# Kernel optimization log

Hardware: AMD Instinct MI355X
Metric: run time of the kernel (lower is better)

Reference implementation:

```python
import jax, jax.numpy as jnp
import numpy as np

K, N, M, D = 64, 8192, 8, 32  # locations, time steps, covariate features, memory depth


def setup_inputs() -> dict:
    key = jax.random.key(0)
    ks = jax.random.split(key, 6)
    obs = jax.random.uniform(ks[0], (K, N), dtype=jnp.float32)            # event counts [K, N]
    covs = jax.random.normal(ks[1], (K, N, M), dtype=jnp.float32)          # covariates  [K, N, M]
    hbeta = jnp.array([2.0], dtype=jnp.float32)                            # decay rate param (torch init: 2)
    halpha = jax.random.uniform(ks[2], (K, K), dtype=jnp.float32) * 0.01   # excitation matrix, U(0, 0.01)
    gamma = jax.random.uniform(ks[3], (K,), dtype=jnp.float32) * 0.01      # covariate gate, U(0, 0.01)
    W1 = jax.random.normal(ks[4], (20, 2 * D * M), dtype=jnp.float32) * 0.05
    b1 = jnp.zeros((20,), dtype=jnp.float32)
    W2 = jax.random.normal(ks[5], (1, 20), dtype=jnp.float32) * 0.05
    b2 = jnp.zeros((1,), dtype=jnp.float32)
    return dict(obs=obs, covs=covs, hbeta=hbeta, halpha=halpha, gamma=gamma,
                W1=W1, b1=b1, W2=W2, b2=b2)


def _forward(obs, covs, hbeta, halpha, gamma, W1, b1, W2, b2):
    k, n = obs.shape
    beta = hbeta[0]
    decay = jnp.exp(-beta)

    # Excitation: S[t] = sum_{tp < t} obs[:, tp] * beta * exp(-(t - tp) * beta)
    # exact O(N) linear recurrence instead of the original per-t O(t) resummation.
    def step(S, o):
        return decay * (S + beta * o), S
    _, S_all = jax.lax.scan(step, jnp.zeros((k,), obs.dtype), obs.T)  # [N, K]
    lam1 = jax.nn.softplus(jnp.einsum('kj,nj->kn', halpha, S_all))     # [K, N] (hmu = 0 in subclass)

    # Edge-padded covariate windows: window at t is padded[:, t : t + 2D, :]
    padded = jnp.concatenate([
        jnp.repeat(covs[:, :1, :], D, axis=1),   # left pad with first step
        covs,
        jnp.repeat(covs[:, -1:, :], D, axis=1),  # right pad with last step
    ], axis=1)                                   # [K, N + 2D, M]
    idx = jnp.arange(n)[:, None] + jnp.arange(2 * D)[None, :]  # [N, 2D]
    X = padded[:, idx, :].reshape(k, n, 2 * D * M)             # [K, N, 2DM], time-major then M (matches torch reshape)

    # Tiny 2-layer MLP with softplus activations, vectorized over (K, N)
    h = jax.nn.softplus(jnp.einsum('knf,hf->knh', X, W1) + b1)           # [K, N, 20]
    mu = jax.nn.softplus(jnp.einsum('knh,oh->kno', h, W2) + b2)[..., 0]  # [K, N]

    lams = lam1 + gamma[:, None] * mu                                    # [K, N]
    loglik = jnp.sum(obs * jnp.log(lams) - lams)
    return loglik, lams


def reference(obs, covs, hbeta, halpha, gamma, W1, b1, W2, b2):
    return _forward(obs, covs, hbeta, halpha, gamma, W1, b1, W2, b2)
```

## Files before the change

kernel.cpp:

```cpp
#include <hip/hip_runtime.h>
#include <hip/hip_bf16.h>
#include <math.h>

#define KL 64
#define NT 8192
#define MF 8
#define DD 32
#define WIN 64
#define HD 20
#define HP 32
#define KF 512
#define NB 256
#define NXB (NT / NB)
#define NBLK (NXB * KL)
#define GRPS (KF / 8)
#define GROW 24
#define W1SZ (GRPS * GROW * 8)

typedef __attribute__((ext_vector_type(8))) short bf16x8;
typedef __attribute__((ext_vector_type(4))) float f32x4;

__device__ __forceinline__ float softplus_f(float x) {
    float e = __expf(-fabsf(x));
    return fmaxf(x, 0.0f) + __logf(1.0f + e);
}
__device__ __forceinline__ short f2bf(float x) {
    __hip_bfloat16 h = __float2bfloat16(x);
    return *reinterpret_cast<short*>(&h);
}

__global__ __launch_bounds__(256)
void pack_kernel(const float* __restrict__ W1, const float* __restrict__ b1,
                 const float* __restrict__ W2, short* __restrict__ W1b,
                 float* __restrict__ b1p, float* __restrict__ W2p) {
    int t = blockIdx.x * 256 + threadIdx.x;
    #pragma unroll
    for (int i = 0; i < 3; ++i) {
        int p = t + i * 4096;
        int e = p & 7;
        int rg = p >> 3;
        int r = rg % GROW;
        int grp = rg / GROW;
        W1b[p] = (r < HD) ? f2bf(W1[r * KF + grp * 8 + e]) : (short)0;
    }
    if (blockIdx.x == 0 && threadIdx.x < HP) {
        b1p[threadIdx.x] = (threadIdx.x < HD) ? b1[threadIdx.x] : 0.0f;
        W2p[threadIdx.x] = (threadIdx.x < HD) ? W2[threadIdx.x] : 0.0f;
    }
}

__global__ __launch_bounds__(256)
void mlp_mfma_kernel(const float* __restrict__ covs, const float* __restrict__ obs,
                     const float* __restrict__ halpha, const float* __restrict__ hbeta,
                     const short* __restrict__ W1b, const float* __restrict__ b1p,
                     const float* __restrict__ W2p, const float* __restrict__ b2,
                     const float* __restrict__ gamma, float* __restrict__ lams,
                     float* __restrict__ partial) {
    __shared__ short cov_s[(NB + WIN) * MF];
    __shared__ float T_s[NB + WIN];
    __shared__ float hsum[NB];
    __shared__ float wred[4];

    int k    = blockIdx.y;
    int n0   = blockIdx.x * NB;
    int tid  = threadIdx.x;
    int lane = tid & 63;
    int wave = tid >> 6;

    int n = n0 + tid;
    size_t idx = (size_t)k * NT + n;
    float obs_n = obs[idx];
    float beta  = hbeta[0];
    float gam   = gamma[k];
    float b2v   = b2[0];

    const float* cbase = covs + (size_t)k * NT * MF;
    for (int row = tid; row < NB + WIN; row += 256) {
        int tt = n0 - DD + row;
        tt = tt < 0 ? 0 : (tt > NT - 1 ? NT - 1 : tt);
        const float4* cp = (const float4*)(cbase + (size_t)tt * MF);
        float4 c0 = cp[0], c1 = cp[1];
        bf16x8 v;
        v[0] = f2bf(c0.x); v[1] = f2bf(c0.y); v[2] = f2bf(c0.z); v[3] = f2bf(c0.w);
        v[4] = f2bf(c1.x); v[5] = f2bf(c1.y); v[6] = f2bf(c1.z); v[7] = f2bf(c1.w);
        *(bf16x8*)&cov_s[row * MF] = v;
    }
    __syncthreads();

    int c = lane & 15;
    int g = lane >> 4;
    int wrow = wave * 64;

    f32x4 acc[4][2];
    #pragma unroll
    for (int mt = 0; mt < 4; ++mt) {
        acc[mt][0] = (f32x4){0.f, 0.f, 0.f, 0.f};
        acc[mt][1] = (f32x4){0.f, 0.f, 0.f, 0.f};
    }

    int r1 = (c < 4) ? (16 + c) : HD;
    const short* pB0 = W1b + g * (GROW * 8) + c * 8;
    const short* pB1 = W1b + g * (GROW * 8) + r1 * 8;
    const short* pA  = &cov_s[(wrow + c + g) * MF];

    const float* arow = halpha + (size_t)k * KL;
    int tA = n0 - WIN + tid;
    tA = tA < 0 ? 0 : tA;
    int tB = n0 + (NB - WIN) + wave * 16 + (lane & 15);
    float aA = 0.0f, aB = 0.0f;

    #pragma unroll 2
    for (int kk = 0; kk < KF / 32; ++kk) {
        #pragma unroll
        for (int jj = 0; jj < 4; ++jj) {
            int j = kk * 4 + jj;
            float aj = arow[j];
            const float* orow = obs + (size_t)j * NT;
            aA = fmaf(aj, orow[tA], aA);
            aB = fmaf(aj, orow[tB], aB);
        }
        bf16x8 b0  = *(const bf16x8*)(pB0 + kk * (4 * GROW * 8));
        bf16x8 b1v = *(const bf16x8*)(pB1 + kk * (4 * GROW * 8));
        #pragma unroll
        for (int mt = 0; mt < 4; ++mt) {
            bf16x8 a = *(const bf16x8*)(pA + (mt * 16 + kk * 4) * MF);
            acc[mt][0] = __builtin_amdgcn_mfma_f32_16x16x32_bf16(a, b0,  acc[mt][0], 0, 0, 0);
            acc[mt][1] = __builtin_amdgcn_mfma_f32_16x16x32_bf16(a, b1v, acc[mt][1], 0, 0, 0);
        }
    }
    T_s[tid] = aA;
    if (lane < 16) T_s[NB + wave * 16 + lane] = aB;

    float w2a = W2p[c],      b1a = b1p[c];
    float w2b = W2p[16 + c], b1b = b1p[16 + c];
    #pragma unroll
    for (int mt = 0; mt < 4; ++mt) {
        float rs[4];
        #pragma unroll
        for (int j = 0; j < 4; ++j) {
            float v = w2a * softplus_f(acc[mt][0][j] + b1a)
                    + w2b * softplus_f(acc[mt][1][j] + b1b);
            v += __shfl_xor(v, 1, 64);
            v += __shfl_xor(v, 2, 64);
            v += __shfl_xor(v, 4, 64);
            v += __shfl_xor(v, 8, 64);
            rs[j] = v;
        }
        if (c == 0)
            *(float4*)&hsum[wrow + mt * 16 + g * 4] = (float4){rs[0], rs[1], rs[2], rs[3]};
    }
    __syncthreads();

    float decay = __expf(-beta);
    int Lmax = (int)(30.0f / beta) + 2;
    float la = 0.0f;
    if (n0 > 0) {
        if (Lmax > WIN) Lmax = WIN;
        int it4 = (Lmax + 3) >> 2;
        float d2 = decay * decay;
        float d4 = d2 * d2;
        float w1 = beta * decay, w2 = w1 * decay, w3 = w2 * decay, w4 = w3 * decay;
        float la0 = 0.f, la1 = 0.f, la2 = 0.f, la3 = 0.f;
        const float* Tp = &T_s[tid + WIN];
        for (int it = 0; it < it4; ++it) {
            int i = it * 4;
            la0 = fmaf(w1, Tp[-(i + 1)], la0); w1 *= d4;
            la1 = fmaf(w2, Tp[-(i + 2)], la1); w2 *= d4;
            la2 = fmaf(w3, Tp[-(i + 3)], la2); w3 *= d4;
            la3 = fmaf(w4, Tp[-(i + 4)], la3); w4 *= d4;
        }
        la = (la0 + la1) + (la2 + la3);
    } else {
        if (Lmax > NT) Lmax = NT;
        float w = beta * decay;
        for (int i = 1; i <= Lmax; ++i) {
            if (i <= n) la = fmaf(w, T_s[tid + WIN - i], la);
            w *= decay;
        }
    }
    float lam1 = softplus_f(la);
    float mu = softplus_f(hsum[tid] + b2v);
    float lam = lam1 + gam * mu;
    lams[idx] = lam;
    float term = fmaf(obs_n, __logf(lam), -lam);

    #pragma unroll
    for (int off = 32; off > 0; off >>= 1) term += __shfl_down(term, off, 64);
    if ((tid & 63) == 0) wred[tid >> 6] = term;
    __syncthreads();
    if (tid == 0)
        partial[blockIdx.y * gridDim.x + blockIdx.x] =
            (wred[0] + wred[1]) + (wred[2] + wred[3]);
}

__global__ __launch_bounds__(256)
void finalize_kernel(const float* __restrict__ partial, float* __restrict__ out0) {
    __shared__ float wred[4];
    int tid = threadIdx.x;
    float s = 0.0f;
    #pragma unroll
    for (int i = 0; i < NBLK / 256; ++i) s += partial[i * 256 + tid];
    #pragma unroll
    for (int off = 32; off > 0; off >>= 1) s += __shfl_down(s, off, 64);
    if ((tid & 63) == 0) wred[tid >> 6] = s;
    __syncthreads();
    if (tid == 0) out0[0] = (wred[0] + wred[1]) + (wred[2] + wred[3]);
}

extern "C" void kernel_launch(void* const* d_in, const int* in_sizes, int n_in,
                              void* d_out, int out_size, void* d_ws, size_t ws_size,
                              hipStream_t stream) {
    const float* obs    = (const float*)d_in[0];
    const float* covs   = (const float*)d_in[1];
    const float* hbeta  = (const float*)d_in[2];
    const float* halpha = (const float*)d_in[3];
    const float* gamma  = (const float*)d_in[4];
    const float* W1     = (const float*)d_in[5];
    const float* b1     = (const float*)d_in[6];
    const float* W2     = (const float*)d_in[7];
    const float* b2     = (const float*)d_in[8];

    float* out  = (float*)d_out;
    float* lams = out + 1;

    char* ws = (char*)d_ws;
    float* partial = (float*)ws;
    float* b1p     = (float*)(ws + 8192);
    float* W2p     = (float*)(ws + 8320);
    short* W1b     = (short*)(ws + 8448);

    dim3 block(256);
    pack_kernel<<<dim3(16), block, 0, stream>>>(W1, b1, W2, W1b, b1p, W2p);
    mlp_mfma_kernel<<<dim3(NXB, KL), block, 0, stream>>>(
        covs, obs, halpha, hbeta, W1b, b1p, W2p, b2, gamma, lams, partial);
    finalize_kernel<<<1, block, 0, stream>>>(partial, out);
}
```

Baseline: 42.67 us.

## Make each wave self-contained to remove block-level barriers

Result: no change. 43.22 us (+1.3%).

```diff
diff --git a/kernel.cpp b/kernel.cpp
--- a/kernel.cpp
+++ b/kernel.cpp
@@ -13,6 +13,7 @@
 #define NB 256
 #define NXB (NT / NB)
 #define NBLK (NXB * KL)
+#define NPART (NBLK * 4)
 #define GRPS (KF / 8)
 #define GROW 24
 #define W1SZ (GRPS * GROW * 8)
@@ -56,18 +57,18 @@
                      const float* __restrict__ W2p, const float* __restrict__ b2,
                      const float* __restrict__ gamma, float* __restrict__ lams,
                      float* __restrict__ partial) {
-    __shared__ short cov_s[(NB + WIN) * MF];
-    __shared__ float T_s[NB + WIN];
-    __shared__ float hsum[NB];
-    __shared__ float wred[4];
+    __shared__ short cov_s[4][128 * MF];
+    __shared__ float T_s[4][128];
+    __shared__ float hsum[4][64];
 
     int k    = blockIdx.y;
     int n0   = blockIdx.x * NB;
     int tid  = threadIdx.x;
     int lane = tid & 63;
     int wave = tid >> 6;
-
-    int n = n0 + tid;
+    int base = n0 + wave * 64;
+
+    int n = base + lane;
     size_t idx = (size_t)k * NT + n;
     float obs_n = obs[idx];
     float beta  = hbeta[0];
@@ -75,21 +76,26 @@
     float b2v   = b2[0];
 
     const float* cbase = covs + (size_t)k * NT * MF;
-    for (int row = tid; row < NB + WIN; row += 256) {
-        int tt = n0 - DD + row;
-        tt = tt < 0 ? 0 : (tt > NT - 1 ? NT - 1 : tt);
-        const float4* cp = (const float4*)(cbase + (size_t)tt * MF);
-        float4 c0 = cp[0], c1 = cp[1];
-        bf16x8 v;
-        v[0] = f2bf(c0.x); v[1] = f2bf(c0.y); v[2] = f2bf(c0.z); v[3] = f2bf(c0.w);
-        v[4] = f2bf(c1.x); v[5] = f2bf(c1.y); v[6] = f2bf(c1.z); v[7] = f2bf(c1.w);
-        *(bf16x8*)&cov_s[row * MF] = v;
-    }
-    __syncthreads();
+    {
+        int t1 = base - DD + lane;
+        t1 = t1 < 0 ? 0 : t1;
+        int t2 = base + DD + lane;
+        t2 = t2 > NT - 1 ? NT - 1 : t2;
+        const float4* cp1 = (const float4*)(cbase + (size_t)t1 * MF);
+        const float4* cp2 = (const float4*)(cbase + (size_t)t2 * MF);
+        float4 a0 = cp1[0], a1 = cp1[1];
+        float4 d0 = cp2[0], d1 = cp2[1];
+        bf16x8 v1, v2;
+        v1[0] = f2bf(a0.x); v1[1] = f2bf(a0.y); v1[2] = f2bf(a0.z); v1[3] = f2bf(a0.w);
+        v1[4] = f2bf(a1.x); v1[5] = f2bf(a1.y); v1[6] = f2bf(a1.z); v1[7] = f2bf(a1.w);
+        v2[0] = f2bf(d0.x); v2[1] = f2bf(d0.y); v2[2] = f2bf(d0.z); v2[3] = f2bf(d0.w);
+        v2[4] = f2bf(d1.x); v2[5] = f2bf(d1.y); v2[6] = f2bf(d1.z); v2[7] = f2bf(d1.w);
+        *(bf16x8*)&cov_s[wave][lane * MF] = v1;
+        *(bf16x8*)&cov_s[wave][(lane + 64) * MF] = v2;
+    }
 
     int c = lane & 15;
     int g = lane >> 4;
-    int wrow = wave * 64;
 
     f32x4 acc[4][2];
     #pragma unroll
@@ -101,12 +107,12 @@
     int r1 = (c < 4) ? (16 + c) : HD;
     const short* pB0 = W1b + g * (GROW * 8) + c * 8;
     const short* pB1 = W1b + g * (GROW * 8) + r1 * 8;
-    const short* pA  = &cov_s[(wrow + c + g) * MF];
+    const short* pA  = &cov_s[wave][(c + g) * MF];
 
     const float* arow = halpha + (size_t)k * KL;
-    int tA = n0 - WIN + tid;
+    int tA = base - WIN + lane;
     tA = tA < 0 ? 0 : tA;
-    int tB = n0 + (NB - WIN) + wave * 16 + (lane & 15);
+    int tB = base + lane;
     float aA = 0.0f, aB = 0.0f;
 
     #pragma unroll 2
@@ -114,10 +120,10 @@
         #pragma unroll
         for (int jj = 0; jj < 4; ++jj) {
             int j = kk * 4 + jj;
-            float aj = arow[j];
+            float ajv = arow[j];
             const float* orow = obs + (size_t)j * NT;
-            aA = fmaf(aj, orow[tA], aA);
-            aB = fmaf(aj, orow[tB], aB);
+            aA = fmaf(ajv, orow[tA], aA);
+            aB = fmaf(ajv, orow[tB], aB);
         }
         bf16x8 b0  = *(const bf16x8*)(pB0 + kk * (4 * GROW * 8));
         bf16x8 b1v = *(const bf16x8*)(pB1 + kk * (4 * GROW * 8));
@@ -128,40 +134,47 @@
             acc[mt][1] = __builtin_amdgcn_mfma_f32_16x16x32_bf16(a, b1v, acc[mt][1], 0, 0, 0);
         }
     }
-    T_s[tid] = aA;
-    if (lane < 16) T_s[NB + wave * 16 + lane] = aB;
+    T_s[wave][lane] = aA;
+    T_s[wave][64 + lane] = aB;
 
     float w2a = W2p[c],      b1a = b1p[c];
     float w2b = W2p[16 + c], b1b = b1p[16 + c];
+    float cur[16];
     #pragma unroll
     for (int mt = 0; mt < 4; ++mt) {
-        float rs[4];
         #pragma unroll
         for (int j = 0; j < 4; ++j) {
-            float v = w2a * softplus_f(acc[mt][0][j] + b1a)
-                    + w2b * softplus_f(acc[mt][1][j] + b1b);
-            v += __shfl_xor(v, 1, 64);
-            v += __shfl_xor(v, 2, 64);
-            v += __shfl_xor(v, 4, 64);
-            v += __shfl_xor(v, 8, 64);
-            rs[j] = v;
-        }
-        if (c == 0)
-            *(float4*)&hsum[wrow + mt * 16 + g * 4] = (float4){rs[0], rs[1], rs[2], rs[3]};
-    }
-    __syncthreads();
+            cur[mt * 4 + j] = w2a * softplus_f(acc[mt][0][j] + b1a)
+                            + w2b * softplus_f(acc[mt][1][j] + b1b);
+        }
+    }
+    #pragma unroll
+    for (int m = 1; m <= 8; m <<= 1) {
+        int half = 8 / m;
+        #pragma unroll
+        for (int s = 0; s < half; ++s) {
+            float x0 = cur[s], x1 = cur[s + half];
+            float t = (lane & m) ? x0 : x1;
+            float u = __shfl_xor(t, m, 64);
+            cur[s] = ((lane & m) ? x1 : x0) + u;
+        }
+    }
+    {
+        int iv = ((c & 1) << 3) | ((c & 2) << 1) | ((c & 4) >> 1) | ((c & 8) >> 3);
+        hsum[wave][(iv >> 2) * 16 + g * 4 + (iv & 3)] = cur[0];
+    }
 
     float decay = __expf(-beta);
     int Lmax = (int)(30.0f / beta) + 2;
+    if (Lmax > WIN) Lmax = WIN;
     float la = 0.0f;
-    if (n0 > 0) {
-        if (Lmax > WIN) Lmax = WIN;
+    const float* Tp = &T_s[wave][64 + lane];
+    if (n >= WIN) {
         int it4 = (Lmax + 3) >> 2;
         float d2 = decay * decay;
         float d4 = d2 * d2;
         float w1 = beta * decay, w2 = w1 * decay, w3 = w2 * decay, w4 = w3 * decay;
         float la0 = 0.f, la1 = 0.f, la2 = 0.f, la3 = 0.f;
-        const float* Tp = &T_s[tid + WIN];
         for (int it = 0; it < it4; ++it) {
             int i = it * 4;
             la0 = fmaf(w1, Tp[-(i + 1)], la0); w1 *= d4;
@@ -171,26 +184,22 @@
         }
         la = (la0 + la1) + (la2 + la3);
     } else {
-        if (Lmax > NT) Lmax = NT;
         float w = beta * decay;
         for (int i = 1; i <= Lmax; ++i) {
-            if (i <= n) la = fmaf(w, T_s[tid + WIN - i], la);
+            if (i <= n) la = fmaf(w, Tp[-i], la);
             w *= decay;
         }
     }
     float lam1 = softplus_f(la);
-    float mu = softplus_f(hsum[tid] + b2v);
+    float mu = softplus_f(hsum[wave][lane] + b2v);
     float lam = lam1 + gam * mu;
     lams[idx] = lam;
     float term = fmaf(obs_n, __logf(lam), -lam);
 
     #pragma unroll
     for (int off = 32; off > 0; off >>= 1) term += __shfl_down(term, off, 64);
-    if ((tid & 63) == 0) wred[tid >> 6] = term;
-    __syncthreads();
-    if (tid == 0)
-        partial[blockIdx.y * gridDim.x + blockIdx.x] =
-            (wred[0] + wred[1]) + (wred[2] + wred[3]);
+    if (lane == 0)
+        partial[((size_t)blockIdx.y * NXB + blockIdx.x) * 4 + wave] = term;
 }
 
 __global__ __launch_bounds__(256)
@@ -199,7 +208,7 @@
     int tid = threadIdx.x;
     float s = 0.0f;
     #pragma unroll
-    for (int i = 0; i < NBLK / 256; ++i) s += partial[i * 256 + tid];
+    for (int i = 0; i < NPART / 256; ++i) s += partial[i * 256 + tid];
     #pragma unroll
     for (int off = 32; off > 0; off >>= 1) s += __shfl_down(s, off, 64);
     if ((tid & 63) == 0) wred[tid >> 6] = s;
@@ -225,9 +234,9 @@
 
     char* ws = (char*)d_ws;
     float* partial = (float*)ws;
-    float* b1p     = (float*)(ws + 8192);
-    float* W2p     = (float*)(ws + 8320);
-    short* W1b     = (short*)(ws + 8448);
+    float* b1p     = (float*)(ws + 32768);
+    float* W2p     = (float*)(ws + 32896);
+    short* W1b     = (short*)(ws + 33024);
 
     dim3 block(256);
     pack_kernel<<<dim3(16), block, 0, stream>>>(W1, b1, W2, W1b, b1p, W2p);
```
